# Optimization experiments

Hardware: AMD Instinct MI355X
Metric: run time of the kernel (lower is better)

The kernel has to match this reference:

```python
import jax, jax.numpy as jnp
import numpy as np


def setup_inputs() -> dict:
    key = jax.random.key(0)
    kq, kk, kv = jax.random.split(key, 3)
    B, S, D = 4, 4096, 128
    q = jax.random.normal(kq, (B, S, D), dtype=jnp.float32)
    k = jax.random.normal(kk, (B, S, D), dtype=jnp.float32)
    v = jax.random.normal(kv, (B, S, D), dtype=jnp.float32)
    return {"q": q, "k": k, "v": v}


def reference(q, k, v):
    # naive scaled dot-product attention: softmax(q k^T / sqrt(d)) v
    scale = 1.0 / jnp.sqrt(jnp.asarray(q.shape[-1], q.dtype))
    scores = jnp.einsum("bsd,btd->bst", q, k) * scale  # [B,S,S]
    probs = jax.nn.softmax(scores, axis=-1)
    out = jnp.einsum("bst,btd->bsd", probs, v)  # [B,S,Dv]
    return out
```

## Files before the change

kernel.cpp:

```cpp
#include <hip/hip_runtime.h>
#include <cmath>
#include <cstdint>

typedef __attribute__((ext_vector_type(8))) __bf16 bf16x8;
typedef __attribute__((ext_vector_type(16))) float f32x16;
typedef unsigned int u32;
typedef unsigned short u16;

constexpr int Bn = 4, Sn = 4096, Dn = 128;
constexpr int OSTR = 132;
constexpr float SCL2E = 0.08838834764831845f * 1.4426950408889634f;

__device__ __forceinline__ u32 pk2(float a, float b) {
  u32 ua = __builtin_bit_cast(u32, a) + 0x8000u;
  u32 ub = __builtin_bit_cast(u32, b) + 0x8000u;
  return __builtin_amdgcn_perm(ub, ua, 0x07060302u);
}

__launch_bounds__(256)
__global__ void prep_kv(const float* __restrict__ Kg, const float* __restrict__ Vg,
                        u16* __restrict__ Kf, u16* __restrict__ Vf) {
  __shared__ float Vl[64 * 132];
  const int kt = blockIdx.x, b = blockIdx.y;
  const int tid = threadIdx.x;
  const size_t tileBase = ((size_t)b * 64 + kt) * 1024;

  #pragma unroll
  for (int r = 0; r < 4; ++r) {
    const int row = (tid >> 4) + r * 16;
    const int chunk = tid & 15;
    const float* src = Kg + ((size_t)b * Sn + kt * 64 + row) * Dn + chunk * 8;
    float4 f0 = *(const float4*)(src);
    float4 f1 = *(const float4*)(src + 4);
    uint4 o;
    o.x = pk2(f0.x, f0.y); o.y = pk2(f0.z, f0.w);
    o.z = pk2(f1.x, f1.y); o.w = pk2(f1.z, f1.w);
    const int c = row & 31, tile = row >> 5, kc = chunk >> 1, h = chunk & 1;
    const int gk = (kc * 4 + tile * 2 + h) * 32 + c;
    *(uint4*)(Kf + (tileBase + gk) * 8) = o;
  }

  #pragma unroll
  for (int r = 0; r < 8; ++r) {
    const int idx = tid + r * 256;
    const int row = idx >> 5, col = (idx & 31) * 4;
    float4 v = *(const float4*)(Vg + ((size_t)b * Sn + kt * 64 + row) * Dn + col);
    *(float4*)(Vl + row * 132 + col) = v;
  }
  __syncthreads();
  #pragma unroll
  for (int r = 0; r < 4; ++r) {
    const int gv = tid + r * 256;
    const int c = gv & 31, h = (gv >> 5) & 1, nt = (gv >> 6) & 3, kc2 = gv >> 8;
    const int key0 = kc2 * 16 + h * 8, dcol = nt * 32 + c;
    float x[8];
    #pragma unroll
    for (int j = 0; j < 8; ++j) x[j] = Vl[(key0 + j) * 132 + dcol];
    uint4 o;
    o.x = pk2(x[0], x[1]); o.y = pk2(x[2], x[3]);
    o.z = pk2(x[4], x[5]); o.w = pk2(x[6], x[7]);
    *(uint4*)(Vf + (tileBase + gv) * 8) = o;
  }
}

__launch_bounds__(256, 2)
__global__ void attn_mfma(const float* __restrict__ qg, const u16* __restrict__ Kf,
                          const u16* __restrict__ Vf, float* __restrict__ Og) {
  __shared__ __align__(16) unsigned char lds[68608];
  float* Oc = (float*)lds;
  float* ml = (float*)(lds + 67584);

  const int tid = threadIdx.x;
  const int kp = tid >> 6, lane = tid & 63;
  const int c = lane & 31, h = lane >> 5;
  const int b = blockIdx.x & 3;
  const int q0 = (blockIdx.x >> 2) * 32;

  const u16* Kb = Kf + ((size_t)b * 64) * 1024 * 8;
  const u16* Vb = Vf + ((size_t)b * 64) * 1024 * 8;

  bf16x8 qf[8];
  {
    const float* Qr = qg + ((size_t)b * Sn + q0 + c) * Dn;
    #pragma unroll
    for (int kc = 0; kc < 8; ++kc) {
      float4 f0 = *(const float4*)(Qr + kc * 16 + h * 8);
      float4 f1 = *(const float4*)(Qr + kc * 16 + h * 8 + 4);
      uint4 t;
      t.x = pk2(f0.x * SCL2E, f0.y * SCL2E);
      t.y = pk2(f0.z * SCL2E, f0.w * SCL2E);
      t.z = pk2(f1.x * SCL2E, f1.y * SCL2E);
      t.w = pk2(f1.z * SCL2E, f1.w * SCL2E);
      qf[kc] = __builtin_bit_cast(bf16x8, t);
    }
  }

  f32x16 accO[4];
  #pragma unroll
  for (int nt = 0; nt < 4; ++nt)
    #pragma unroll
    for (int r = 0; r < 16; ++r) accO[nt][r] = 0.f;
  float l_i = 0.f;

  #pragma unroll 1
  for (int t8 = 0; t8 < 16; ++t8) {
    const int kt = kp * 16 + t8;
    const u16* Kt = Kb + (size_t)kt * 1024 * 8;
    const u16* Vt = Vb + (size_t)kt * 1024 * 8;

    f32x16 sa0, sa1;
    #pragma unroll
    for (int r = 0; r < 16; ++r) { sa0[r] = 0.f; sa1[r] = 0.f; }
    #pragma unroll
    for (int kc = 0; kc < 8; ++kc) {
      uint4 a0 = *(const uint4*)(Kt + (size_t)((kc * 4 + 0 + h) * 32 + c) * 8);
      uint4 a1 = *(const uint4*)(Kt + (size_t)((kc * 4 + 2 + h) * 32 + c) * 8);
      sa0 = __builtin_amdgcn_mfma_f32_32x32x16_bf16(__builtin_bit_cast(bf16x8, a0), qf[kc], sa0, 0, 0, 0);
      sa1 = __builtin_amdgcn_mfma_f32_32x32x16_bf16(__builtin_bit_cast(bf16x8, a1), qf[kc], sa1, 0, 0, 0);
    }

    float rs = 0.f;
    #pragma unroll
    for (int r = 0; r < 16; ++r) { sa0[r] = exp2f(sa0[r]); rs += sa0[r]; }
    #pragma unroll
    for (int r = 0; r < 16; ++r) { sa1[r] = exp2f(sa1[r]); rs += sa1[r]; }
    rs += __shfl_xor(rs, 32);
    l_i += rs;

    u32 pk2v[2][8];
    #pragma unroll
    for (int i = 0; i < 8; ++i) {
      pk2v[0][i] = pk2(sa0[2 * i], sa0[2 * i + 1]);
      pk2v[1][i] = pk2(sa1[2 * i], sa1[2 * i + 1]);
    }

    #pragma unroll
    for (int kc2 = 0; kc2 < 4; ++kc2) {
      const int t = kc2 >> 1;
      const int bb = (kc2 & 1) * 4;
      u32 o0 = pk2v[t][bb], o1 = pk2v[t][bb + 1], o2 = pk2v[t][bb + 2], o3 = pk2v[t][bb + 3];
      u32 r0 = (u32)__shfl_xor((int)o0, 32);
      u32 r1 = (u32)__shfl_xor((int)o1, 32);
      u32 r2 = (u32)__shfl_xor((int)o2, 32);
      u32 r3 = (u32)__shfl_xor((int)o3, 32);
      uint4 afi;
      afi.x = h ? r2 : o0;
      afi.y = h ? r3 : o1;
      afi.z = h ? o2 : r0;
      afi.w = h ? o3 : r1;
      bf16x8 af = __builtin_bit_cast(bf16x8, afi);
      #pragma unroll
      for (int nt = 0; nt < 4; ++nt) {
        uint4 av = *(const uint4*)(Vt + (size_t)((kc2 * 8 + nt * 2 + h) * 32 + c) * 8);
        accO[nt] = __builtin_amdgcn_mfma_f32_32x32x16_bf16(__builtin_bit_cast(bf16x8, av), af, accO[nt], 0, 0, 0);
      }
    }
  }

  __syncthreads();
  {
    float* od = Oc + (size_t)(kp * 32) * OSTR;
    #pragma unroll
    for (int nt = 0; nt < 4; ++nt)
      #pragma unroll
      for (int r = 0; r < 16; ++r) {
        const int dr = (r & 3) + 8 * (r >> 2) + 4 * h;
        od[c * OSTR + nt * 32 + dr] = accO[nt][r];
      }
    if (h == 0) ml[kp * 32 + c] = l_i;
  }
  __syncthreads();
  {
    const int row = tid >> 3;
    const int d0 = (tid & 7) * 16;
    float lsum = 0.f;
    #pragma unroll
    for (int k2 = 0; k2 < 4; ++k2) lsum += ml[k2 * 32 + row];
    const float inv = 1.f / lsum;
    float4 acc[4];
    #pragma unroll
    for (int j = 0; j < 4; ++j) acc[j] = float4{0.f, 0.f, 0.f, 0.f};
    #pragma unroll
    for (int k2 = 0; k2 < 4; ++k2) {
      const float* oc = Oc + (size_t)(k2 * 32 + row) * OSTR + d0;
      #pragma unroll
      for (int j = 0; j < 4; ++j) {
        float4 vv = *(const float4*)(oc + 4 * j);
        acc[j].x += vv.x; acc[j].y += vv.y;
        acc[j].z += vv.z; acc[j].w += vv.w;
      }
    }
    float* op = Og + ((size_t)b * Sn + q0 + row) * Dn + d0;
    #pragma unroll
    for (int j = 0; j < 4; ++j) {
      float4 o = {acc[j].x * inv, acc[j].y * inv, acc[j].z * inv, acc[j].w * inv};
      *(float4*)(op + 4 * j) = o;
    }
  }
}

extern "C" void kernel_launch(void* const* d_in, const int* in_sizes, int n_in,
                              void* d_out, int out_size, void* d_ws, size_t ws_size,
                              hipStream_t stream) {
  const float* q = (const float*)d_in[0];
  const float* k = (const float*)d_in[1];
  const float* v = (const float*)d_in[2];
  float* out = (float*)d_out;
  const size_t N = (size_t)Bn * Sn * Dn;
  u16* Kf = (u16*)d_ws;
  u16* Vf = Kf + N;

  prep_kv<<<dim3(Sn / 64, Bn), dim3(256), 0, stream>>>(k, v, Kf, Vf);
  attn_mfma<<<dim3((Sn / 32) * Bn), dim3(256), 0, stream>>>(q, Kf, Vf, out);
}
```

Before: 124.7 us.

## Split key range across eight waves and use native bf16 pack and permlane swap

Each block grows to 512 threads, so eight waves each cover eight key tiles instead of four waves covering sixteen. Partial outputs are combined in a two-phase LDS reduction. The float-to-bf16 packing now uses the v_cvt_pk_bf16_f32 instruction, and the cross-half shuffles are replaced by v_permlane32_swap, cutting VALU and LDS-permute work in the inner loop. The change brings more waves and latency hiding per query tile, at the cost of extra reduction and sync overhead and tighter register limits from launch bounds of 512 threads with 4 blocks.

```diff
diff --git a/kernel.cpp b/kernel.cpp
--- a/kernel.cpp
+++ b/kernel.cpp
@@ -12,9 +12,13 @@
 constexpr float SCL2E = 0.08838834764831845f * 1.4426950408889634f;
 
 __device__ __forceinline__ u32 pk2(float a, float b) {
-  u32 ua = __builtin_bit_cast(u32, a) + 0x8000u;
-  u32 ub = __builtin_bit_cast(u32, b) + 0x8000u;
-  return __builtin_amdgcn_perm(ub, ua, 0x07060302u);
+  u32 r;
+  asm("v_cvt_pk_bf16_f32 %0, %1, %2" : "=v"(r) : "v"(a), "v"(b));
+  return r;
+}
+
+__device__ __forceinline__ void pl32swap(u32& a, u32& b) {
+  asm("v_permlane32_swap_b32 %0, %1" : "+v"(a), "+v"(b));
 }
 
 __launch_bounds__(256)
@@ -63,7 +67,7 @@
   }
 }
 
-__launch_bounds__(256, 2)
+__launch_bounds__(512, 4)
 __global__ void attn_mfma(const float* __restrict__ qg, const u16* __restrict__ Kf,
                           const u16* __restrict__ Vf, float* __restrict__ Og) {
   __shared__ __align__(16) unsigned char lds[68608];
@@ -103,8 +107,8 @@
   float l_i = 0.f;
 
   #pragma unroll 1
-  for (int t8 = 0; t8 < 16; ++t8) {
-    const int kt = kp * 16 + t8;
+  for (int t8 = 0; t8 < 8; ++t8) {
+    const int kt = kp * 8 + t8;
     const u16* Kt = Kb + (size_t)kt * 1024 * 8;
     const u16* Vt = Vb + (size_t)kt * 1024 * 8;
 
@@ -138,16 +142,10 @@
     for (int kc2 = 0; kc2 < 4; ++kc2) {
       const int t = kc2 >> 1;
       const int bb = (kc2 & 1) * 4;
-      u32 o0 = pk2v[t][bb], o1 = pk2v[t][bb + 1], o2 = pk2v[t][bb + 2], o3 = pk2v[t][bb + 3];
-      u32 r0 = (u32)__shfl_xor((int)o0, 32);
-      u32 r1 = (u32)__shfl_xor((int)o1, 32);
-      u32 r2 = (u32)__shfl_xor((int)o2, 32);
-      u32 r3 = (u32)__shfl_xor((int)o3, 32);
-      uint4 afi;
-      afi.x = h ? r2 : o0;
-      afi.y = h ? r3 : o1;
-      afi.z = h ? o2 : r0;
-      afi.w = h ? o3 : r1;
+      u32 x0 = pk2v[t][bb], x1 = pk2v[t][bb + 1], x2 = pk2v[t][bb + 2], x3 = pk2v[t][bb + 3];
+      pl32swap(x0, x2);
+      pl32swap(x1, x3);
+      uint4 afi; afi.x = x0; afi.y = x1; afi.z = x2; afi.w = x3;
       bf16x8 af = __builtin_bit_cast(bf16x8, afi);
       #pragma unroll
       for (int nt = 0; nt < 4; ++nt) {
@@ -157,45 +155,52 @@
     }
   }
 
+  float* od = Oc + ((size_t)((kp & 3) * 32) + c) * OSTR + 4 * h;
+  if (kp >= 4) {
+    #pragma unroll
+    for (int nt = 0; nt < 4; ++nt)
+      #pragma unroll
+      for (int qq = 0; qq < 4; ++qq) {
+        float4 w = {accO[nt][4 * qq + 0], accO[nt][4 * qq + 1],
+                    accO[nt][4 * qq + 2], accO[nt][4 * qq + 3]};
+        *(float4*)(od + nt * 32 + 8 * qq) = w;
+      }
+  }
+  if (h == 0) ml[kp * 32 + c] = l_i;
+  __syncthreads();
+  if (kp < 4) {
+    #pragma unroll
+    for (int nt = 0; nt < 4; ++nt)
+      #pragma unroll
+      for (int qq = 0; qq < 4; ++qq) {
+        float4 p = *(const float4*)(od + nt * 32 + 8 * qq);
+        float4 w = {accO[nt][4 * qq + 0] + p.x, accO[nt][4 * qq + 1] + p.y,
+                    accO[nt][4 * qq + 2] + p.z, accO[nt][4 * qq + 3] + p.w};
+        *(float4*)(od + nt * 32 + 8 * qq) = w;
+      }
+  }
   __syncthreads();
   {
-    float* od = Oc + (size_t)(kp * 32) * OSTR;
-    #pragma unroll
-    for (int nt = 0; nt < 4; ++nt)
-      #pragma unroll
-      for (int r = 0; r < 16; ++r) {
-        const int dr = (r & 3) + 8 * (r >> 2) + 4 * h;
-        od[c * OSTR + nt * 32 + dr] = accO[nt][r];
-      }
-    if (h == 0) ml[kp * 32 + c] = l_i;
-  }
-  __syncthreads();
-  {
-    const int row = tid >> 3;
-    const int d0 = (tid & 7) * 16;
+    const int row = tid >> 4;
+    const int d0 = (tid & 15) * 8;
     float lsum = 0.f;
     #pragma unroll
-    for (int k2 = 0; k2 < 4; ++k2) lsum += ml[k2 * 32 + row];
+    for (int k2 = 0; k2 < 8; ++k2) lsum += ml[k2 * 32 + row];
     const float inv = 1.f / lsum;
-    float4 acc[4];
-    #pragma unroll
-    for (int j = 0; j < 4; ++j) acc[j] = float4{0.f, 0.f, 0.f, 0.f};
+    float a[8] = {0.f, 0.f, 0.f, 0.f, 0.f, 0.f, 0.f, 0.f};
     #pragma unroll
     for (int k2 = 0; k2 < 4; ++k2) {
       const float* oc = Oc + (size_t)(k2 * 32 + row) * OSTR + d0;
-      #pragma unroll
-      for (int j = 0; j < 4; ++j) {
-        float4 vv = *(const float4*)(oc + 4 * j);
-        acc[j].x += vv.x; acc[j].y += vv.y;
-        acc[j].z += vv.z; acc[j].w += vv.w;
-      }
+      float4 v0 = *(const float4*)(oc);
+      float4 v1 = *(const float4*)(oc + 4);
+      a[0] += v0.x; a[1] += v0.y; a[2] += v0.z; a[3] += v0.w;
+      a[4] += v1.x; a[5] += v1.y; a[6] += v1.z; a[7] += v1.w;
     }
     float* op = Og + ((size_t)b * Sn + q0 + row) * Dn + d0;
-    #pragma unroll
-    for (int j = 0; j < 4; ++j) {
-      float4 o = {acc[j].x * inv, acc[j].y * inv, acc[j].z * inv, acc[j].w * inv};
-      *(float4*)(op + 4 * j) = o;
-    }
+    float4 o0 = {a[0] * inv, a[1] * inv, a[2] * inv, a[3] * inv};
+    float4 o1 = {a[4] * inv, a[5] * inv, a[6] * inv, a[7] * inv};
+    *(float4*)(op) = o0;
+    *(float4*)(op + 4) = o1;
   }
 }
 
@@ -211,5 +216,5 @@
   u16* Vf = Kf + N;
 
   prep_kv<<<dim3(Sn / 64, Bn), dim3(256), 0, stream>>>(k, v, Kf, Vf);
-  attn_mfma<<<dim3((Sn / 32) * Bn), dim3(256), 0, stream>>>(q, Kf, Vf, out);
-}
+  attn_mfma<<<dim3((Sn / 32) * Bn), dim3(512), 0, stream>>>(q, Kf, Vf, out);
+}
```

Measured after the change: 210.2 us. +68.6%, slower.
